# Kernel optimization log

Hardware: AMD Instinct MI355X
Metric: run time of the kernel (lower is better)

The kernel has to match this reference:

```python
import jax, jax.numpy as jnp
import numpy as np

N_HEADS = 16
ROPE_BASE = 10000.0


def _rope_tables(T, head_dim, dtype):
    d2 = head_dim // 2
    inv_freq = 1.0 / (ROPE_BASE ** (jnp.arange(0, head_dim, 2, dtype=jnp.float32) / head_dim))
    t = jnp.arange(T, dtype=jnp.float32)
    freqs = jnp.outer(t, inv_freq)  # [T, d2]
    cos = jnp.cos(freqs)[None, :, None, :].astype(dtype)  # [1,T,1,d2]
    sin = jnp.sin(freqs)[None, :, None, :].astype(dtype)
    return cos, sin


def _apply_rotary(x, cos, sin):
    # x: [B,T,H,D]; rotate halves
    d = x.shape[-1] // 2
    x1, x2 = x[..., :d], x[..., d:]
    return jnp.concatenate([x1 * cos + x2 * sin, -x1 * sin + x2 * cos], axis=-1)


def setup_inputs() -> dict:
    key = jax.random.key(0)
    k1, k2, k3 = jax.random.split(key, 3)
    B, T, C = 2, 2048, 1024
    x = jax.random.normal(k1, (B, T, C), dtype=jnp.float32)
    w_attn = jax.random.normal(k2, (3 * C, C), dtype=jnp.float32) * (1.0 / np.sqrt(C))
    w_proj = jax.random.normal(k3, (C, C), dtype=jnp.float32) * (1.0 / np.sqrt(C))
    return {"x": x, "w_attn": w_attn, "w_proj": w_proj}


def reference(x, w_attn, w_proj):
    B, T, C = x.shape
    H = N_HEADS
    D = C // H
    qkv = jnp.einsum('btc,fc->btf', x, w_attn)  # [B,T,3C]
    q, k, v = jnp.split(qkv, 3, axis=2)
    q = q.reshape(B, T, H, D)
    k = k.reshape(B, T, H, D)
    v = v.reshape(B, T, H, D)
    cos, sin = _rope_tables(T, D, x.dtype)
    q = _apply_rotary(q, cos, sin)
    k = _apply_rotary(k, cos, sin)
    # causal SDPA, scale 1/sqrt(D)
    scale = 1.0 / np.sqrt(D)
    scores = jnp.einsum('bqhd,bkhd->bhqk', q, k) * scale
    causal = jnp.tril(jnp.ones((T, T), dtype=bool))
    scores = jnp.where(causal[None, None], scores, jnp.finfo(scores.dtype).min)
    attn = jax.nn.softmax(scores, axis=-1)
    y = jnp.einsum('bhqk,bkhd->bqhd', attn, v).reshape(B, T, C)
    return jnp.einsum('btc,oc->bto', y, w_proj)
```

## Files before the change

kernel.cpp:

```cpp
#include <hip/hip_runtime.h>
#include <math.h>

typedef __bf16 bf16x8 __attribute__((ext_vector_type(8)));
typedef float f32x4 __attribute__((ext_vector_type(4)));

__device__ __forceinline__ unsigned f2bf(float f) {
    union { float f; unsigned u; } v; v.f = f;
    return (v.u + 0x7FFFu + ((v.u >> 16) & 1u)) >> 16;
}

__device__ __forceinline__ unsigned cvtpk(float a, float b) {
    unsigned r;
    __asm__("v_cvt_pk_bf16_f32 %0, %1, %2" : "=v"(r) : "v"(a), "v"(b));
    return r;
}

__device__ __forceinline__ void gload16(const ushort* g, ushort* l) {
    __builtin_amdgcn_global_load_lds(
        (const __attribute__((address_space(1))) void*)g,
        (__attribute__((address_space(3))) void*)l, 16, 0, 0);
}

__device__ __forceinline__ bool src_is_fp32(const unsigned* s) {
    int sane = 0;
#pragma unroll
    for (int i = 0; i < 64; ++i) {
        unsigned lo = s[i] & 0xFFFFu;
        unsigned e = (lo >> 7) & 0xFF;
        if (lo == 0u || (e >= 100u && e <= 140u)) sane++;
    }
    return sane < 48;
}

__global__ __launch_bounds__(256) void tobf16_all_kernel(
    const unsigned* __restrict__ s0, const unsigned* __restrict__ s1,
    const unsigned* __restrict__ s2,
    ushort* __restrict__ d0, ushort* __restrict__ d1, ushort* __restrict__ d2) {
    const int bx = blockIdx.x;
    const unsigned* src;
    ushort* dst;
    int lb;
    if (bx < 2048)      { src = s0; dst = d0; lb = bx; }
    else if (bx < 3584) { src = s1; dst = d1; lb = bx - 2048; }
    else                { src = s2; dst = d2; lb = bx - 3584; }
    const int i = lb * 2048 + threadIdx.x * 8;
    if (src_is_fp32(src)) {
        const float* fs = (const float*)src;
        float4 f0 = *(const float4*)(fs + i);
        float4 f1 = *(const float4*)(fs + i + 4);
        uint4 o;
        o.x = f2bf(f0.x) | (f2bf(f0.y) << 16);
        o.y = f2bf(f0.z) | (f2bf(f0.w) << 16);
        o.z = f2bf(f1.x) | (f2bf(f1.y) << 16);
        o.w = f2bf(f1.z) | (f2bf(f1.w) << 16);
        *(uint4*)(dst + i) = o;
    } else {
        *(uint4*)(dst + i) = *(const uint4*)((const ushort*)src + i);
    }
}

constexpr int GBM = 128, GBN = 128, GBK = 32;

__global__ __launch_bounds__(256) void gemm_qkv_rope_kernel(
    const ushort* __restrict__ A, const ushort* __restrict__ Bmat,
    ushort* __restrict__ qkvh, int K) {
    __shared__ ushort As[2][GBM * GBK];
    __shared__ ushort Bs[2][GBN * GBK];

    const int tid  = threadIdx.x;
    const int lane = tid & 63;
    const int wv   = tid >> 6;
    const int wm   = (wv >> 1) * 64;
    const int wn   = (wv & 1) * 64;

    const ushort* Ab = A + (size_t)blockIdx.x * GBM * K;
    const ushort* Bb = Bmat + (size_t)blockIdx.y * GBN * K;

    f32x4 acc[4][4];
#pragma unroll
    for (int i = 0; i < 4; i++)
#pragma unroll
        for (int j = 0; j < 4; j++) acc[i][j] = (f32x4){0.f, 0.f, 0.f, 0.f};

    const int srow = tid >> 2;
    const int scol = (tid & 3) * 8;
    const int fr = lane & 15;
    const int fk = (lane >> 4) * 8;
    const int nK = K >> 5;

    gload16(Ab + (size_t)srow * K + scol,        As[0] + wv * 512);
    gload16(Ab + (size_t)(srow + 64) * K + scol, As[0] + wv * 512 + 2048);
    gload16(Bb + (size_t)srow * K + scol,        Bs[0] + wv * 512);
    gload16(Bb + (size_t)(srow + 64) * K + scol, Bs[0] + wv * 512 + 2048);

#pragma unroll 1
    for (int it = 0; it < nK; ++it) {
        const int cur = it & 1;
        __syncthreads();
        if (it + 1 < nK) {
            const int k0 = (it + 1) << 5, nxt = cur ^ 1;
            gload16(Ab + (size_t)srow * K + k0 + scol,        As[nxt] + wv * 512);
            gload16(Ab + (size_t)(srow + 64) * K + k0 + scol, As[nxt] + wv * 512 + 2048);
            gload16(Bb + (size_t)srow * K + k0 + scol,        Bs[nxt] + wv * 512);
            gload16(Bb + (size_t)(srow + 64) * K + k0 + scol, Bs[nxt] + wv * 512 + 2048);
        }
        bf16x8 af[4], bfr[4];
#pragma unroll
        for (int i = 0; i < 4; i++)
            af[i] = *(const bf16x8*)(As[cur] + (wm + i * 16 + fr) * GBK + fk);
#pragma unroll
        for (int j = 0; j < 4; j++)
            bfr[j] = *(const bf16x8*)(Bs[cur] + (wn + j * 16 + fr) * GBK + fk);
#pragma unroll
        for (int i = 0; i < 4; i++)
#pragma unroll
            for (int j = 0; j < 4; j++)
                acc[i][j] = __builtin_amdgcn_mfma_f32_16x16x32_bf16(af[i], bfr[j], acc[i][j], 0, 0, 0);
    }

    const int crow0 = (lane >> 4) * 4;
    const int col0  = blockIdx.y * GBN + wn;
    const int which = col0 >> 10;
    const int hh    = (col0 >> 6) & 15;

    if (which < 2) {
        ushort* outp = qkvh + (size_t)which * 4194304 + (size_t)hh * 131072;
        const float inva = exp2f((float)fr * -0.41524101186f);
        const float invb = exp2f((float)(fr + 16) * -0.41524101186f);
        const float qs = (which == 0) ? 0.125f : 1.0f;
#pragma unroll
        for (int i = 0; i < 4; i++)
#pragma unroll
            for (int r = 0; r < 4; r++) {
                int row = blockIdx.x * GBM + wm + i * 16 + crow0 + r;
                int t = row & 2047;
                size_t ob = ((size_t)(row >> 11)) * 2097152 + (size_t)t * 64;
                float sa, ca, sb, cb;
                __sincosf((float)t * inva, &sa, &ca);
                __sincosf((float)t * invb, &sb, &cb);
                float q0 = acc[i][0][r], q1 = acc[i][1][r];
                float q2 = acc[i][2][r], q3 = acc[i][3][r];
                float n0 = (q0 * ca + q2 * sa) * qs;
                float n1 = (q1 * cb + q3 * sb) * qs;
                float n2 = (q2 * ca - q0 * sa) * qs;
                float n3 = (q3 * cb - q1 * sb) * qs;
                unsigned u01 = cvtpk(n0, n1);
                unsigned u23 = cvtpk(n2, n3);
                outp[ob + fr]      = (ushort)(u01 & 0xFFFFu);
                outp[ob + 16 + fr] = (ushort)(u01 >> 16);
                outp[ob + 32 + fr] = (ushort)(u23 & 0xFFFFu);
                outp[ob + 48 + fr] = (ushort)(u23 >> 16);
            }
    } else {
        const int row0 = blockIdx.x * GBM;
        ushort* vout = qkvh + (size_t)2 * 4194304
                     + ((size_t)(row0 >> 11)) * 2097152 + (size_t)hh * 131072;
#pragma unroll
        for (int i = 0; i < 4; i++) {
            const int t0 = (blockIdx.x * GBM + wm + i * 16 + crow0) & 2047;
#pragma unroll
            for (int j = 0; j < 4; j++) {
                uint2 u;
                u.x = cvtpk(acc[i][j][0], acc[i][j][1]);
                u.y = cvtpk(acc[i][j][2], acc[i][j][3]);
                *(uint2*)(vout + (size_t)(j * 16 + fr) * 2048 + t0) = u;
            }
        }
    }
}

__global__ __launch_bounds__(256) void gemm_bt_kernel(
    const ushort* __restrict__ A, const ushort* __restrict__ Bmat,
    float* __restrict__ C, int M, int N, int K) {
    __shared__ ushort As[2][GBM * GBK];
    __shared__ ushort Bs[2][GBN * GBK];

    const int tid  = threadIdx.x;
    const int lane = tid & 63;
    const int wv   = tid >> 6;
    const int wm   = (wv >> 1) * 64;
    const int wn   = (wv & 1) * 64;

    const ushort* Ab = A + (size_t)blockIdx.x * GBM * K;
    const ushort* Bb = Bmat + (size_t)blockIdx.y * GBN * K;

    f32x4 acc[4][4];
#pragma unroll
    for (int i = 0; i < 4; i++)
#pragma unroll
        for (int j = 0; j < 4; j++) acc[i][j] = (f32x4){0.f, 0.f, 0.f, 0.f};

    const int srow = tid >> 2;
    const int scol = (tid & 3) * 8;
    const int fr = lane & 15;
    const int fk = (lane >> 4) * 8;
    const int nK = K >> 5;

    gload16(Ab + (size_t)srow * K + scol,        As[0] + wv * 512);
    gload16(Ab + (size_t)(srow + 64) * K + scol, As[0] + wv * 512 + 2048);
    gload16(Bb + (size_t)srow * K + scol,        Bs[0] + wv * 512);
    gload16(Bb + (size_t)(srow + 64) * K + scol, Bs[0] + wv * 512 + 2048);

#pragma unroll 1
    for (int it = 0; it < nK; ++it) {
        const int cur = it & 1;
        __syncthreads();
        if (it + 1 < nK) {
            const int k0 = (it + 1) << 5, nxt = cur ^ 1;
            gload16(Ab + (size_t)srow * K + k0 + scol,        As[nxt] + wv * 512);
            gload16(Ab + (size_t)(srow + 64) * K + k0 + scol, As[nxt] + wv * 512 + 2048);
            gload16(Bb + (size_t)srow * K + k0 + scol,        Bs[nxt] + wv * 512);
            gload16(Bb + (size_t)(srow + 64) * K + k0 + scol, Bs[nxt] + wv * 512 + 2048);
        }
        bf16x8 af[4], bfr[4];
#pragma unroll
        for (int i = 0; i < 4; i++)
            af[i] = *(const bf16x8*)(As[cur] + (wm + i * 16 + fr) * GBK + fk);
#pragma unroll
        for (int j = 0; j < 4; j++)
            bfr[j] = *(const bf16x8*)(Bs[cur] + (wn + j * 16 + fr) * GBK + fk);
#pragma unroll
        for (int i = 0; i < 4; i++)
#pragma unroll
            for (int j = 0; j < 4; j++)
                acc[i][j] = __builtin_amdgcn_mfma_f32_16x16x32_bf16(af[i], bfr[j], acc[i][j], 0, 0, 0);
    }

    const int crow0 = (lane >> 4) * 4;
#pragma unroll
    for (int i = 0; i < 4; i++)
#pragma unroll
        for (int j = 0; j < 4; j++)
#pragma unroll
            for (int r = 0; r < 4; r++) {
                int row = blockIdx.x * GBM + wm + i * 16 + crow0 + r;
                int col = blockIdx.y * GBN + wn + j * 16 + fr;
                C[(size_t)row * N + col] = acc[i][j][r];
            }
}

#define NEG_BIG (-1e30f)
constexpr int LPP    = 72;
constexpr int VT_OFF = 16384;
constexpr int PS_OFF = 32768;

__global__ __launch_bounds__(512) void attn_kernel(const ushort* __restrict__ qkvh,
                                                   ushort* __restrict__ y) {
    __shared__ ushort SM[PS_OFF + 8 * 32 * LPP];

    const int tid  = threadIdx.x;
    const int lane = tid & 63;
    const int wv   = tid >> 6;
    const int half = wv >> 2;
    const int wq   = wv & 3;
    const int jb   = half * 4;

    const int id   = blockIdx.x + (blockIdx.y << 3);
    const int xcd  = id & 7;
    const int k8   = id >> 3;
    const int bh   = xcd * 4 + (k8 & 3);
    const int pid  = k8 >> 2;
    const int b    = bh >> 4, h = bh & 15;

    const ushort* qp = qkvh + (size_t)b * 2097152 + (size_t)h * 131072;
    const ushort* kp = qp + 4194304;
    const ushort* vp = qp + 8388608;

    const int fr = lane & 15;
    const int fq = lane >> 4;
    const int fk = fq * 8;

    const int ksrcA = (tid >> 3) * 64 + (((tid & 7) ^ ((tid >> 3) & 7)) << 3);
    const int ksrcB = ksrcA + 4096;
    const int vsrcA = (tid >> 4) * 2048 + (((tid & 15) ^ ((tid >> 4) & 15)) << 3);
    const int vsrcB = vsrcA + 65536;
    const int koff0 = (fq ^ (fr & 7)) << 3;
    const int koff1 = koff0 ^ 32;
    const int voff0 = ((half * 8 + fq) ^ fr) << 3;
    const int voff1 = ((half * 8 + 4 + fq) ^ fr) << 3;

    ushort* pw = SM + PS_OFF + wv * (32 * LPP);

#pragma unroll 1
    for (int seg = 0; seg < 2; ++seg) {
        const int qb = seg ? (15 - pid) : pid;
        const int nIt = qb + 1;

        __syncthreads();

        gload16(kp + ksrcA, SM + wv * 512);
        gload16(kp + ksrcB, SM + 4096 + wv * 512);
        gload16(vp + vsrcA, SM + VT_OFF + wv * 512);
        gload16(vp + vsrcB, SM + VT_OFF + 4096 + wv * 512);

        const int qrowA = qb * 128 + wq * 32 + fr;
        bf16x8 qfA0 = *(const bf16x8*)(qp + (size_t)qrowA * 64 + fk);
        bf16x8 qfA1 = *(const bf16x8*)(qp + (size_t)qrowA * 64 + 32 + fk);
        bf16x8 qfB0 = *(const bf16x8*)(qp + (size_t)(qrowA + 16) * 64 + fk);
        bf16x8 qfB1 = *(const bf16x8*)(qp + (size_t)(qrowA + 16) * 64 + 32 + fk);

        f32x4 oA[4], oB[4];
#pragma unroll
        for (int j4 = 0; j4 < 4; ++j4) {
            oA[j4] = (f32x4){0.f, 0.f, 0.f, 0.f};
            oB[j4] = (f32x4){0.f, 0.f, 0.f, 0.f};
        }
        float lsumA = 0.f, lsumB = 0.f;

#pragma unroll 1
        for (int it = 0; it < nIt; ++it) {
            const int cur = it & 1;
            const int k0 = it * 128;
            const ushort* Ksc = SM + cur * 8192;
            const ushort* Vtc = SM + VT_OFF + cur * 8192;
            __syncthreads();
            if (it + 1 < nIt) {
                const int nxt = cur ^ 1;
                gload16(kp + (it + 1) * 8192 + ksrcA, SM + nxt * 8192 + wv * 512);
                gload16(kp + (it + 1) * 8192 + ksrcB, SM + nxt * 8192 + 4096 + wv * 512);
                gload16(vp + (it + 1) * 128 + vsrcA, SM + VT_OFF + nxt * 8192 + wv * 512);
                gload16(vp + (it + 1) * 128 + vsrcB, SM + VT_OFF + nxt * 8192 + 4096 + wv * 512);
            }

            f32x4 sA[4], sB[4];
#pragma unroll
            for (int jl = 0; jl < 4; ++jl) {
                const int row = ((jb + jl) * 16 + fr) * 64;
                bf16x8 kf0 = *(const bf16x8*)(Ksc + row + koff0);
                bf16x8 kf1 = *(const bf16x8*)(Ksc + row + koff1);
                f32x4 zA = (f32x4){0.f, 0.f, 0.f, 0.f};
                f32x4 zB = (f32x4){0.f, 0.f, 0.f, 0.f};
                zA = __builtin_amdgcn_mfma_f32_16x16x32_bf16(kf0, qfA0, zA, 0, 0, 0);
                zA = __builtin_amdgcn_mfma_f32_16x16x32_bf16(kf1, qfA1, zA, 0, 0, 0);
                zB = __builtin_amdgcn_mfma_f32_16x16x32_bf16(kf0, qfB0, zB, 0, 0, 0);
                zB = __builtin_amdgcn_mfma_f32_16x16x32_bf16(kf1, qfB1, zB, 0, 0, 0);
                sA[jl] = zA;
                sB[jl] = zB;
            }
            if (it + 1 < nIt) {
#pragma unroll
                for (int jl = 0; jl < 4; ++jl)
#pragma unroll
                    for (int r = 0; r < 4; ++r) {
                        float pA = __expf(sA[jl][r]);
                        float pB = __expf(sB[jl][r]);
                        sA[jl][r] = pA; lsumA += pA;
                        sB[jl][r] = pB; lsumB += pB;
                    }
            } else {
#pragma unroll
                for (int jl = 0; jl < 4; ++jl)
#pragma unroll
                    for (int r = 0; r < 4; ++r) {
                        const int key = k0 + (jb + jl) * 16 + fq * 4 + r;
                        float vA = (key > qrowA)      ? NEG_BIG : sA[jl][r];
                        float vB = (key > qrowA + 16) ? NEG_BIG : sB[jl][r];
                        float pA = __expf(vA);
                        float pB = __expf(vB);
                        sA[jl][r] = pA; lsumA += pA;
                        sB[jl][r] = pB; lsumB += pB;
                    }
            }

#pragma unroll
            for (int jl = 0; jl < 4; ++jl) {
                uint2 uA, uB;
                uA.x = cvtpk(sA[jl][0], sA[jl][1]);
                uA.y = cvtpk(sA[jl][2], sA[jl][3]);
                uB.x = cvtpk(sB[jl][0], sB[jl][1]);
                uB.y = cvtpk(sB[jl][2], sB[jl][3]);
                *(uint2*)(pw + fr * LPP + jl * 16 + fq * 4)        = uA;
                *(uint2*)(pw + (16 + fr) * LPP + jl * 16 + fq * 4) = uB;
            }
            __asm__ volatile("" ::: "memory");

#pragma unroll
            for (int kl = 0; kl < 2; ++kl) {
                bf16x8 pfA = *(const bf16x8*)(pw + fr * LPP + kl * 32 + fk);
                bf16x8 pfB = *(const bf16x8*)(pw + (16 + fr) * LPP + kl * 32 + fk);
                const int voff = kl ? voff1 : voff0;
#pragma unroll
                for (int j4 = 0; j4 < 4; ++j4) {
                    bf16x8 vf = *(const bf16x8*)(Vtc + (j4 * 16 + fr) * 128 + voff);
                    oA[j4] = __builtin_amdgcn_mfma_f32_16x16x32_bf16(pfA, vf, oA[j4], 0, 0, 0);
                    oB[j4] = __builtin_amdgcn_mfma_f32_16x16x32_bf16(pfB, vf, oB[j4], 0, 0, 0);
                }
            }
        }

        lsumA += __shfl_xor(lsumA, 16, 64);
        lsumA += __shfl_xor(lsumA, 32, 64);
        lsumB += __shfl_xor(lsumB, 16, 64);
        lsumB += __shfl_xor(lsumB, 32, 64);

        __syncthreads();
        float* exA = (float*)(SM + PS_OFF) + (wq * 2) * 1104;
        float* exB = exA + 1104;
        if (half) {
#pragma unroll
            for (int j4 = 0; j4 < 4; ++j4)
#pragma unroll
                for (int r = 0; r < 4; ++r) {
                    exA[lane * 17 + j4 * 4 + r] = oA[j4][r];
                    exB[lane * 17 + j4 * 4 + r] = oB[j4][r];
                }
            if (fq == 0) {
                exA[1088 + fr] = lsumA;
                exB[1088 + fr] = lsumB;
            }
        }
        __syncthreads();
        if (!half) {
            float linvA[4], linvB[4];
#pragma unroll
            for (int r = 0; r < 4; ++r) {
                float ownA = __shfl(lsumA, fq * 4 + r, 64);
                float ownB = __shfl(lsumB, fq * 4 + r, 64);
                linvA[r] = 1.0f / (ownA + exA[1088 + fq * 4 + r]);
                linvB[r] = 1.0f / (ownB + exB[1088 + fq * 4 + r]);
            }
#pragma unroll
            for (int j4 = 0; j4 < 4; j4 += 2)
#pragma unroll
                for (int r = 0; r < 4; ++r) {
                    int rowA = qb * 128 + wq * 32 + fq * 4 + r;
                    size_t ybA = ((size_t)b * 2048 + rowA) * 1024 + h * 64;
                    float a0 = (oA[j4][r]     + exA[lane * 17 + j4 * 4 + r])       * linvA[r];
                    float a1 = (oA[j4 + 1][r] + exA[lane * 17 + (j4 + 1) * 4 + r]) * linvA[r];
                    unsigned ua = cvtpk(a0, a1);
                    y[ybA + j4 * 16 + fr]       = (ushort)(ua & 0xFFFFu);
                    y[ybA + (j4 + 1) * 16 + fr] = (ushort)(ua >> 16);

                    size_t ybB = ybA + (size_t)16 * 1024;
                    float b0 = (oB[j4][r]     + exB[lane * 17 + j4 * 4 + r])       * linvB[r];
                    float b1 = (oB[j4 + 1][r] + exB[lane * 17 + (j4 + 1) * 4 + r]) * linvB[r];
                    unsigned ub = cvtpk(b0, b1);
                    y[ybB + j4 * 16 + fr]       = (ushort)(ub & 0xFFFFu);
                    y[ybB + (j4 + 1) * 16 + fr] = (ushort)(ub >> 16);
                }
        }
    }
}

extern "C" void kernel_launch(void* const* d_in, const int* in_sizes, int n_in,
                              void* d_out, int out_size, void* d_ws, size_t ws_size,
                              hipStream_t stream) {
    const int nx = in_sizes[0];
    const int na = in_sizes[1];
    const int np = in_sizes[2];

    ushort* qkvh = (ushort*)d_ws;
    ushort* yb   = qkvh + (size_t)3 * 4194304;
    ushort* xb   = yb + (size_t)4096 * 1024;
    ushort* wab  = xb + nx;
    ushort* wpb  = wab + na;
    size_t need = ((size_t)3 * 4194304 + (size_t)4096 * 1024 + nx + na + np) * 2;
    if (ws_size < need) return;

    tobf16_all_kernel<<<dim3(4096), 256, 0, stream>>>(
        (const unsigned*)d_in[0], (const unsigned*)d_in[1], (const unsigned*)d_in[2],
        xb, wab, wpb);

    gemm_qkv_rope_kernel<<<dim3(32, 24), 256, 0, stream>>>(xb, wab, qkvh, 1024);
    attn_kernel<<<dim3(8, 32), 512, 0, stream>>>(qkvh, yb);
    gemm_bt_kernel<<<dim3(32, 8), 256, 0, stream>>>(yb, wpb, (float*)d_out, 4096, 1024, 1024);
}
```

Before: 179.1 us.

## Load K/V fragments directly from global memory instead of LDS staging

```diff
diff --git a/kernel.cpp b/kernel.cpp
--- a/kernel.cpp
+++ b/kernel.cpp
@@ -240,13 +240,11 @@
 }
 
 #define NEG_BIG (-1e30f)
-constexpr int LPP    = 72;
-constexpr int VT_OFF = 16384;
-constexpr int PS_OFF = 32768;
+constexpr int LPP = 72;
 
 __global__ __launch_bounds__(512) void attn_kernel(const ushort* __restrict__ qkvh,
                                                    ushort* __restrict__ y) {
-    __shared__ ushort SM[PS_OFF + 8 * 32 * LPP];
+    __shared__ ushort SM[8 * 32 * LPP];
 
     const int tid  = threadIdx.x;
     const int lane = tid & 63;
@@ -270,16 +268,7 @@
     const int fq = lane >> 4;
     const int fk = fq * 8;
 
-    const int ksrcA = (tid >> 3) * 64 + (((tid & 7) ^ ((tid >> 3) & 7)) << 3);
-    const int ksrcB = ksrcA + 4096;
-    const int vsrcA = (tid >> 4) * 2048 + (((tid & 15) ^ ((tid >> 4) & 15)) << 3);
-    const int vsrcB = vsrcA + 65536;
-    const int koff0 = (fq ^ (fr & 7)) << 3;
-    const int koff1 = koff0 ^ 32;
-    const int voff0 = ((half * 8 + fq) ^ fr) << 3;
-    const int voff1 = ((half * 8 + 4 + fq) ^ fr) << 3;
-
-    ushort* pw = SM + PS_OFF + wv * (32 * LPP);
+    ushort* pw = SM + wv * (32 * LPP);
 
 #pragma unroll 1
     for (int seg = 0; seg < 2; ++seg) {
@@ -287,11 +276,6 @@
         const int nIt = qb + 1;
 
         __syncthreads();
-
-        gload16(kp + ksrcA, SM + wv * 512);
-        gload16(kp + ksrcB, SM + 4096 + wv * 512);
-        gload16(vp + vsrcA, SM + VT_OFF + wv * 512);
-        gload16(vp + vsrcB, SM + VT_OFF + 4096 + wv * 512);
 
         const int qrowA = qb * 128 + wq * 32 + fr;
         bf16x8 qfA0 = *(const bf16x8*)(qp + (size_t)qrowA * 64 + fk);
@@ -309,35 +293,38 @@
 
 #pragma unroll 1
         for (int it = 0; it < nIt; ++it) {
-            const int cur = it & 1;
             const int k0 = it * 128;
-            const ushort* Ksc = SM + cur * 8192;
-            const ushort* Vtc = SM + VT_OFF + cur * 8192;
-            __syncthreads();
-            if (it + 1 < nIt) {
-                const int nxt = cur ^ 1;
-                gload16(kp + (it + 1) * 8192 + ksrcA, SM + nxt * 8192 + wv * 512);
-                gload16(kp + (it + 1) * 8192 + ksrcB, SM + nxt * 8192 + 4096 + wv * 512);
-                gload16(vp + (it + 1) * 128 + vsrcA, SM + VT_OFF + nxt * 8192 + wv * 512);
-                gload16(vp + (it + 1) * 128 + vsrcB, SM + VT_OFF + nxt * 8192 + 4096 + wv * 512);
-            }
+            const bool lastIt = (it + 1 == nIt);
+            if (lastIt && half && (wq < 2)) continue;
+
+            bf16x8 kf0[4], kf1[4];
+#pragma unroll
+            for (int jl = 0; jl < 4; ++jl) {
+                const size_t krow = (size_t)(k0 + (jb + jl) * 16 + fr) * 64;
+                kf0[jl] = *(const bf16x8*)(kp + krow + fk);
+                kf1[jl] = *(const bf16x8*)(kp + krow + 32 + fk);
+            }
+            bf16x8 vf[2][4];
+#pragma unroll
+            for (int kl = 0; kl < 2; ++kl)
+#pragma unroll
+                for (int j4 = 0; j4 < 4; ++j4)
+                    vf[kl][j4] = *(const bf16x8*)(vp + (size_t)(j4 * 16 + fr) * 2048
+                                                  + k0 + half * 64 + kl * 32 + fk);
 
             f32x4 sA[4], sB[4];
 #pragma unroll
             for (int jl = 0; jl < 4; ++jl) {
-                const int row = ((jb + jl) * 16 + fr) * 64;
-                bf16x8 kf0 = *(const bf16x8*)(Ksc + row + koff0);
-                bf16x8 kf1 = *(const bf16x8*)(Ksc + row + koff1);
                 f32x4 zA = (f32x4){0.f, 0.f, 0.f, 0.f};
                 f32x4 zB = (f32x4){0.f, 0.f, 0.f, 0.f};
-                zA = __builtin_amdgcn_mfma_f32_16x16x32_bf16(kf0, qfA0, zA, 0, 0, 0);
-                zA = __builtin_amdgcn_mfma_f32_16x16x32_bf16(kf1, qfA1, zA, 0, 0, 0);
-                zB = __builtin_amdgcn_mfma_f32_16x16x32_bf16(kf0, qfB0, zB, 0, 0, 0);
-                zB = __builtin_amdgcn_mfma_f32_16x16x32_bf16(kf1, qfB1, zB, 0, 0, 0);
+                zA = __builtin_amdgcn_mfma_f32_16x16x32_bf16(kf0[jl], qfA0, zA, 0, 0, 0);
+                zA = __builtin_amdgcn_mfma_f32_16x16x32_bf16(kf1[jl], qfA1, zA, 0, 0, 0);
+                zB = __builtin_amdgcn_mfma_f32_16x16x32_bf16(kf0[jl], qfB0, zB, 0, 0, 0);
+                zB = __builtin_amdgcn_mfma_f32_16x16x32_bf16(kf1[jl], qfB1, zB, 0, 0, 0);
                 sA[jl] = zA;
                 sB[jl] = zB;
             }
-            if (it + 1 < nIt) {
+            if (!lastIt) {
 #pragma unroll
                 for (int jl = 0; jl < 4; ++jl)
 #pragma unroll
@@ -378,12 +365,10 @@
             for (int kl = 0; kl < 2; ++kl) {
                 bf16x8 pfA = *(const bf16x8*)(pw + fr * LPP + kl * 32 + fk);
                 bf16x8 pfB = *(const bf16x8*)(pw + (16 + fr) * LPP + kl * 32 + fk);
-                const int voff = kl ? voff1 : voff0;
 #pragma unroll
                 for (int j4 = 0; j4 < 4; ++j4) {
-                    bf16x8 vf = *(const bf16x8*)(Vtc + (j4 * 16 + fr) * 128 + voff);
-                    oA[j4] = __builtin_amdgcn_mfma_f32_16x16x32_bf16(pfA, vf, oA[j4], 0, 0, 0);
-                    oB[j4] = __builtin_amdgcn_mfma_f32_16x16x32_bf16(pfB, vf, oB[j4], 0, 0, 0);
+                    oA[j4] = __builtin_amdgcn_mfma_f32_16x16x32_bf16(pfA, vf[kl][j4], oA[j4], 0, 0, 0);
+                    oB[j4] = __builtin_amdgcn_mfma_f32_16x16x32_bf16(pfB, vf[kl][j4], oB[j4], 0, 0, 0);
                 }
             }
         }
@@ -394,7 +379,7 @@
         lsumB += __shfl_xor(lsumB, 32, 64);
 
         __syncthreads();
-        float* exA = (float*)(SM + PS_OFF) + (wq * 2) * 1104;
+        float* exA = (float*)SM + (wq * 2) * 1104;
         float* exB = exA + 1104;
         if (half) {
 #pragma unroll
```

Result: slower. 211.5 us (+18.1%).
